# Kernel optimization log

Measured on AMD Instinct MI355X. Metric: run time of the kernel, lower is better.

The kernel has to match this reference:

```python
import jax, jax.numpy as jnp
import numpy as np

EPS = 1e-8  # EPSILON in original repo (sharpen denom); cosine eps matches torch default 1e-8
MAX_SHIFT = 1
M_FEAT = 128


def _lstm_cell(x, h, c, W_ih, W_hh, b_ih, b_hh):
    gates = x @ W_ih.T + b_ih + h @ W_hh.T + b_hh
    i, f, g, o = jnp.split(gates, 4, axis=1)
    c_new = jax.nn.sigmoid(f) * c + jax.nn.sigmoid(i) * jnp.tanh(g)
    h_new = jax.nn.sigmoid(o) * jnp.tanh(c_new)
    return h_new, c_new


def _content_address(bank, k, b):
    # torch cosine_similarity over dim 2: dot / max(|m||k|, eps)
    dot = jnp.einsum('bnm,bm->bn', bank, k)
    denom = jnp.maximum(jnp.linalg.norm(bank, axis=2) * jnp.linalg.norm(k, axis=1, keepdims=True), 1e-8)
    return jax.nn.softmax(b * dot / denom, axis=1)


def _shift(w, s):
    # circular unroll then valid cross-correlation with per-batch kernel s [B, 2*MAX_SHIFT+1]
    wp = jnp.concatenate([w[:, -MAX_SHIFT:], w, w[:, :MAX_SHIFT]], axis=1)
    N = w.shape[1]
    taps = 2 * MAX_SHIFT + 1
    return sum(s[:, i:i + 1] * wp[:, i:i + N] for i in range(taps))


def _sharpen(w, r):
    wr = w ** r
    return wr / (wr.sum(axis=1, keepdims=True) + EPS)


def _move(bank, w_prev, k, b, g, s, r):
    w = _content_address(bank, k, b)
    w = w + (1.0 - g) * w_prev  # faithful: w_c is NOT scaled by g in the source
    w = _shift(w, s)
    return _sharpen(w, r)


def _split_read(p):
    M = M_FEAT
    k = p[:, :M]
    b = jax.nn.softplus(p[:, M:M + 1])
    g = jax.nn.sigmoid(p[:, M + 1:M + 2])
    s = jax.nn.softmax(p[:, M + 2:M + 5], axis=1)
    r = 1.0 + jax.nn.softplus(p[:, M + 5:M + 6])
    return k, b, g, s, r


def _split_write(p):
    M = M_FEAT
    k, b, g, s, r = _split_read(p[:, :M + 6])
    e = jax.nn.sigmoid(p[:, M + 6:M + 6 + M])
    a = p[:, M + 6 + M:M + 6 + 2 * M]
    return k, b, g, s, r, e, a


def setup_inputs() -> dict:
    key = jax.random.key(0)
    ks = jax.random.split(key, 16)
    B, E, H, N, M, O = 64, 256, 512, 4096, 128, 256
    rd_out, wr_out = M + 2 * MAX_SHIFT + 4, 3 * M + 2 * MAX_SHIFT + 4
    sc = 0.05
    return {
        'x': jax.random.normal(ks[0], (B, E), jnp.float32),
        'h_prev': jax.random.normal(ks[1], (B, H), jnp.float32),
        'c_prev': jax.random.normal(ks[2], (B, H), jnp.float32),
        'bank': jax.random.normal(ks[3], (B, N, M), jnp.float32) * 0.1,
        'read_w_prev': jnp.zeros((3, B, N), jnp.float32),
        'write_w_prev': jnp.zeros((3, B, N), jnp.float32),
        'W_ih': jax.random.normal(ks[4], (4 * H, E), jnp.float32) * sc,
        'W_hh': jax.random.normal(ks[5], (4 * H, H), jnp.float32) * sc,
        'b_ih': jax.random.normal(ks[6], (4 * H,), jnp.float32) * sc,
        'b_hh': jax.random.normal(ks[7], (4 * H,), jnp.float32) * sc,
        'read_W': jax.random.normal(ks[8], (3, rd_out, H), jnp.float32) * sc,
        'read_b': jax.random.normal(ks[9], (3, rd_out), jnp.float32) * sc,
        'write_W': jax.random.normal(ks[10], (3, wr_out, H), jnp.float32) * sc,
        'write_b': jax.random.normal(ks[11], (3, wr_out), jnp.float32) * sc,
        'out_W': jax.random.normal(ks[12], (O, 3 * M + H), jnp.float32) * sc,
        'out_b': jax.random.normal(ks[13], (O,), jnp.float32) * sc,
    }


def reference(x, h_prev, c_prev, bank, read_w_prev, write_w_prev,
              W_ih, W_hh, b_ih, b_hh, read_W, read_b, write_W, write_b,
              out_W, out_b):
    h, c = _lstm_cell(x, h_prev, c_prev, W_ih, W_hh, b_ih, b_hh)
    reads = []
    for i in range(3):  # head_num=3, structurally distinct params per head
        # write head: update bank
        pw = h @ write_W[i].T + write_b[i]
        k, b, g, s, r, e, a = _split_write(pw)
        ww = _move(bank, write_w_prev[i], k, b, g, s, r)
        bank = bank * (1.0 - ww[:, :, None] * e[:, None, :]) + ww[:, :, None] * a[:, None, :]
        # read head: read from updated bank
        pr = h @ read_W[i].T + read_b[i]
        k, b, g, s, r = _split_read(pr)
        wr = _move(bank, read_w_prev[i], k, b, g, s, r)
        reads.append(jnp.einsum('bn,bnm->bm', wr, bank))
    out = jnp.concatenate(reads + [h], axis=1) @ out_W.T + out_b
    return out
```

## Files before the change

### kernel.cpp

```cpp
#include <hip/hip_runtime.h>
#include <math.h>

namespace {

constexpr int kB = 64;
constexpr int kN = 4096;
constexpr int kM = 128;
constexpr int kH = 512;
constexpr int kE = 256;
constexpr int kO = 256;
constexpr int kGates = 4 * kH;
constexpr int kCatW = 3 * kM + kH;
constexpr int kPRow = 1600;
constexpr int kWN = kB * kN;
constexpr int GRID = 256;
constexpr int TPB = 512;
constexpr float kLog2e = 1.4426950408889634f;

__device__ __forceinline__ float sigm_(float x) { return 1.f / (1.f + expf(-x)); }
__device__ __forceinline__ float softplus_(float x) { return x > 20.f ? x : log1pf(expf(x)); }

struct Args {
  const float *x, *h_prev, *c_prev, *bank, *read_w_prev, *write_w_prev;
  const float *W_ih, *W_hh, *b_ih, *b_hh, *read_W, *read_b, *write_W, *write_b, *out_W, *out_b;
  float *out;
  float *gates0, *gates1, *praw0, *praw1, *cat;
  float *kwb, *krb, *evb, *avb, *scal, *sdot;
  float *wp0, *wp1, *wp2, *wp3, *wp4, *wp5;
  float *mA, *mB;
  unsigned *cnt;
};

union SMem {
  struct { float At[64 * 20]; float Wt[64 * 65]; } g;
  struct { float hs[256 * 18]; float Wt[64 * 65]; } p;
  struct { float wb[kN]; float red[8]; } a;
  struct { float nred[4][2]; } s;
  struct { float rl[2 * kM]; } r;
  struct { float As[64 * 72]; float Ws[64 * 72]; } o;
};

__device__ __forceinline__ void gsync(unsigned* cnt, unsigned target) {
  __syncthreads();
  if (threadIdx.x == 0) {
    __builtin_amdgcn_fence(__ATOMIC_RELEASE, "agent");
    __hip_atomic_fetch_add(cnt, 1u, __ATOMIC_RELAXED, __HIP_MEMORY_SCOPE_AGENT);
    while (__hip_atomic_load(cnt, __ATOMIC_RELAXED, __HIP_MEMORY_SCOPE_AGENT) < target)
      __builtin_amdgcn_s_sleep(1);
    __builtin_amdgcn_fence(__ATOMIC_ACQUIRE, "agent");
  }
  __syncthreads();
}

__device__ void addr_core8(int tid, float* loc, const float* sc, const float* __restrict__ wp,
                           float* wb, float* red) {
  const float g = sc[1], r = sc[2];
  const float s0 = sc[3], s1c = sc[4], s2 = sc[5];
  const int lane = tid & 63, wid = tid >> 6;
  __syncthreads();
  float mx = loc[0];
#pragma unroll
  for (int i = 1; i < 8; i++) mx = fmaxf(mx, loc[i]);
#pragma unroll
  for (int m = 1; m < 64; m <<= 1) mx = fmaxf(mx, __shfl_xor(mx, m, 64));
  if (lane == 0) red[wid] = mx;
  __syncthreads();
  mx = red[0];
#pragma unroll
  for (int k = 1; k < 8; k++) mx = fmaxf(mx, red[k]);
  float sum = 0.f;
#pragma unroll
  for (int i = 0; i < 8; i++) { loc[i] = exp2f((loc[i] - mx) * kLog2e); sum += loc[i]; }
#pragma unroll
  for (int m = 1; m < 64; m <<= 1) sum += __shfl_xor(sum, m, 64);
  __syncthreads();
  if (lane == 0) red[wid] = sum;
  __syncthreads();
  sum = red[0];
#pragma unroll
  for (int k = 1; k < 8; k++) sum += red[k];
  const float inv = 1.f / sum;
  const float omg = 1.f - g;
#pragma unroll
  for (int i = 0; i < 8; i++) {
    int n = tid + i * TPB;
    wb[n] = loc[i] * inv + omg * wp[n];
  }
  __syncthreads();
  float ssum = 0.f;
#pragma unroll
  for (int i = 0; i < 8; i++) {
    int n = tid + i * TPB;
    float sh = s0 * wb[(n + kN - 1) & (kN - 1)] + s1c * wb[n] + s2 * wb[(n + 1) & (kN - 1)];
    float y = (sh > 0.f) ? exp2f(r * log2f(sh)) : 0.f;
    loc[i] = y;
    ssum += y;
  }
#pragma unroll
  for (int m = 1; m < 64; m <<= 1) ssum += __shfl_xor(ssum, m, 64);
  __syncthreads();
  if (lane == 0) red[wid] = ssum;
  __syncthreads();
  ssum = red[0];
#pragma unroll
  for (int k = 1; k < 8; k++) ssum += red[k];
  const float invs = 1.f / (ssum + 1e-8f);
#pragma unroll
  for (int i = 0; i < 8; i++) loc[i] *= invs;
  __syncthreads();
}

__global__ __launch_bounds__(TPB, 2) void mega(Args P) {
  const int bid = blockIdx.x;
  const int tid = threadIdx.x;
  __shared__ SMem sm;

  {
    const int khalf = bid >> 7;
    const int unit = bid & 127;
    const int b0 = (unit >> 5) * 16;
    const int j0 = (unit & 31) * 64;
    const int jg = tid & 63;
    const int bq2 = (tid >> 6) * 2;
    float acc0 = 0.f, acc1 = 0.f;
    for (int kc6 = 0; kc6 < 6; kc6++) {
      const int kc = khalf * 6 + kc6;
      const bool isx = kc < 4;
      const float* A = isx ? P.x : P.h_prev;
      const float* W = isx ? P.W_ih : P.W_hh;
      const int lda = isx ? kE : kH;
      const int k0 = (isx ? kc : (kc - 4)) * 64;
      __syncthreads();
      {
        int bb = tid >> 5;
        int kk = (tid & 31) * 2;
        float2 v = *(const float2*)(A + (size_t)(b0 + bb) * lda + k0 + kk);
        sm.g.At[(kk + 0) * 20 + bb] = v.x;
        sm.g.At[(kk + 1) * 20 + bb] = v.y;
      }
#pragma unroll
      for (int i = 0; i < 2; i++) {
        int idx = tid + i * 512;
        int jj = idx >> 4;
        int kk = (idx & 15) * 4;
        float4 w = *(const float4*)(W + (size_t)(j0 + jj) * lda + k0 + kk);
        sm.g.Wt[(kk + 0) * 65 + jj] = w.x; sm.g.Wt[(kk + 1) * 65 + jj] = w.y;
        sm.g.Wt[(kk + 2) * 65 + jj] = w.z; sm.g.Wt[(kk + 3) * 65 + jj] = w.w;
      }
      __syncthreads();
#pragma unroll 4
      for (int k = 0; k < 64; k++) {
        float2 av = *(const float2*)&sm.g.At[k * 20 + bq2];
        float wv = sm.g.Wt[k * 65 + jg];
        acc0 += av.x * wv; acc1 += av.y * wv;
      }
    }
    float* gd = khalf ? P.gates1 : P.gates0;
    gd[(size_t)(b0 + bq2 + 0) * kGates + j0 + jg] = acc0;
    gd[(size_t)(b0 + bq2 + 1) * kGates + j0 + jg] = acc1;
  }
  gsync(P.cnt, GRID * 1);

  if (bid < 200) {
    const int kh = bid / 100;
    const int u = bid % 100;
    const int b0 = (u / 25) * 16;
    const int jt = u % 25;
    const int j0 = jt * 64;
    const int kbase = kh * 256;
    for (int i = tid; i < 16 * 256; i += TPB) {
      int bb = i >> 8, kl = i & 255;
      int kk = kbase + kl;
      int b = b0 + bb;
      const float* g0 = P.gates0 + (size_t)b * kGates;
      const float* g1 = P.gates1 + (size_t)b * kGates;
      float i_ = g0[kk]        + g1[kk]        + P.b_ih[kk]        + P.b_hh[kk];
      float f_ = g0[512 + kk]  + g1[512 + kk]  + P.b_ih[512 + kk]  + P.b_hh[512 + kk];
      float gg = g0[1024 + kk] + g1[1024 + kk] + P.b_ih[1024 + kk] + P.b_hh[1024 + kk];
      float o_ = g0[1536 + kk] + g1[1536 + kk] + P.b_ih[1536 + kk] + P.b_hh[1536 + kk];
      float c = sigm_(f_) * P.c_prev[(size_t)b * kH + kk] + sigm_(i_) * tanhf(gg);
      float h = sigm_(o_) * tanhf(c);
      sm.p.hs[kl * 18 + bb] = h;
      if (jt == 0) P.cat[(size_t)b * kCatW + 3 * kM + kk] = h;
    }
    const int jg = tid & 63;
    const int bq2 = (tid >> 6) * 2;
    float acc0 = 0.f, acc1 = 0.f;
    for (int kc = 0; kc < 4; kc++) {
      const int k0 = kbase + kc * 64;
      const int kl0 = kc * 64;
      __syncthreads();
#pragma unroll
      for (int i = 0; i < 2; i++) {
        int idx = tid + i * 512;
        int jj = idx >> 4;
        int kk = (idx & 15) * 4;
        int j = j0 + jj;
        float4 w = make_float4(0.f, 0.f, 0.f, 0.f);
        if (j < 1170)      w = *(const float4*)(P.write_W + (size_t)j * kH + k0 + kk);
        else if (j < 1572) w = *(const float4*)(P.read_W + (size_t)(j - 1170) * kH + k0 + kk);
        sm.p.Wt[(kk + 0) * 65 + jj] = w.x; sm.p.Wt[(kk + 1) * 65 + jj] = w.y;
        sm.p.Wt[(kk + 2) * 65 + jj] = w.z; sm.p.Wt[(kk + 3) * 65 + jj] = w.w;
      }
      __syncthreads();
#pragma unroll 4
      for (int k = 0; k < 64; k++) {
        float2 av = *(const float2*)&sm.p.hs[(kl0 + k) * 18 + bq2];
        float wv = sm.p.Wt[k * 65 + jg];
        acc0 += av.x * wv; acc1 += av.y * wv;
      }
    }
    float* pd = kh ? P.praw1 : P.praw0;
    if (j0 + jg < 1572) {
      pd[(size_t)(b0 + bq2 + 0) * kPRow + j0 + jg] = acc0;
      pd[(size_t)(b0 + bq2 + 1) * kPRow + j0 + jg] = acc1;
    }
  } else if (bid < 216) {
#pragma unroll
    for (int q = 0; q < 2; q++) {
      int i = (bid - 200) * 1024 + tid + q * 512;
      P.out[i] = P.out_b[i & (kO - 1)];
    }
  } else if (bid < 232) {
#pragma unroll
    for (int q = 0; q < 3; q++) {
      int i = (bid - 216) * 1536 + tid + q * 512;
      P.cat[(size_t)(i / 384) * kCatW + (i % 384)] = 0.f;
    }
  }
  gsync(P.cnt, GRID * 2);

  if (bid < kB) {
    const int b = bid;
    const int m = tid & 127;
    const int hg = tid >> 7;
    const float* pr0 = P.praw0 + (size_t)b * kPRow;
    const float* pr1 = P.praw1 + (size_t)b * kPRow;
    {
      const bool isw = hg < 3;
      const int base = isw ? hg * 390 : 1170;
      const float* bias = isw ? (P.write_b + hg * 390) : P.read_b;
      const int slot = isw ? hg : 3;
      float kv = pr0[base + m] + pr1[base + m] + bias[m];
      if (isw) {
        P.kwb[((size_t)hg * kB + b) * kM + m] = kv;
        P.evb[((size_t)hg * kB + b) * kM + m] =
            sigm_(pr0[base + 134 + m] + pr1[base + 134 + m] + bias[134 + m]);
        P.avb[((size_t)hg * kB + b) * kM + m] =
            pr0[base + 262 + m] + pr1[base + 262 + m] + bias[262 + m];
      } else {
        P.krb[((size_t)0 * kB + b) * kM + m] = kv;
      }
      float sq = kv * kv;
#pragma unroll
      for (int mm = 1; mm < 64; mm <<= 1) sq += __shfl_xor(sq, mm, 64);
      if ((tid & 63) == 0) sm.s.nred[hg][m >> 6] = sq;
      __syncthreads();
      if (m == 0) {
        float* s = P.scal + ((size_t)slot * kB + b) * 8;
        s[0] = softplus_(pr0[base + 128] + pr1[base + 128] + bias[128]);
        s[1] = sigm_(pr0[base + 129] + pr1[base + 129] + bias[129]);
        s[2] = 1.f + softplus_(pr0[base + 133] + pr1[base + 133] + bias[133]);
        float x0 = pr0[base + 130] + pr1[base + 130] + bias[130];
        float x1 = pr0[base + 131] + pr1[base + 131] + bias[131];
        float x2 = pr0[base + 132] + pr1[base + 132] + bias[132];
        float mx = fmaxf(x0, fmaxf(x1, x2));
        float e0 = expf(x0 - mx), e1 = expf(x1 - mx), e2 = expf(x2 - mx);
        float si = 1.f / (e0 + e1 + e2);
        s[3] = e0 * si; s[4] = e1 * si; s[5] = e2 * si;
        s[6] = sqrtf(sm.s.nred[hg][0] + sm.s.nred[hg][1]);
      }
      __syncthreads();
    }
    {
      const int j = (hg < 2) ? hg + 1 : 2;
      const bool act = hg < 2;
      const int base = 1170 + j * 134;
      const float* bias = P.read_b + j * 134;
      const int slot = 3 + j;
      float kv = pr0[base + m] + pr1[base + m] + bias[m];
      if (act) P.krb[((size_t)j * kB + b) * kM + m] = kv;
      float sq = kv * kv;
#pragma unroll
      for (int mm = 1; mm < 64; mm <<= 1) sq += __shfl_xor(sq, mm, 64);
      if ((tid & 63) == 0) sm.s.nred[hg][m >> 6] = sq;
      __syncthreads();
      if (m == 0 && act) {
        float* s = P.scal + ((size_t)slot * kB + b) * 8;
        s[0] = softplus_(pr0[base + 128] + pr1[base + 128] + bias[128]);
        s[1] = sigm_(pr0[base + 129] + pr1[base + 129] + bias[129]);
        s[2] = 1.f + softplus_(pr0[base + 133] + pr1[base + 133] + bias[133]);
        float x0 = pr0[base + 130] + pr1[base + 130] + bias[130];
        float x1 = pr0[base + 131] + pr1[base + 131] + bias[131];
        float x2 = pr0[base + 132] + pr1[base + 132] + bias[132];
        float mx = fmaxf(x0, fmaxf(x1, x2));
        float e0 = expf(x0 - mx), e1 = expf(x1 - mx), e2 = expf(x2 - mx);
        float si = 1.f / (e0 + e1 + e2);
        s[3] = e0 * si; s[4] = e1 * si; s[5] = e2 * si;
        s[6] = sqrtf(sm.s.nred[hg][0] + sm.s.nred[hg][1]);
      }
      __syncthreads();
    }
    if (tid < 64) {
      const float* a0v = P.avb + ((size_t)0 * kB + b) * kM;
      const float* a2v = P.avb + ((size_t)2 * kB + b) * kM;
      const float* u[5] = {a0v, a0v, a0v, a2v, a2v};
      const float* v[5] = {P.krb + ((size_t)0 * kB + b) * kM,
                           P.kwb + ((size_t)1 * kB + b) * kM,
                           a0v,
                           P.krb + ((size_t)2 * kB + b) * kM,
                           a2v};
#pragma unroll
      for (int d = 0; d < 5; d++) {
        float s = u[d][tid] * v[d][tid] + u[d][tid + 64] * v[d][tid + 64];
#pragma unroll
        for (int mm = 1; mm < 64; mm <<= 1) s += __shfl_xor(s, mm, 64);
        if (tid == 0) P.sdot[b * 8 + d] = s;
      }
    }
  }
  gsync(P.cnt, GRID * 3);

  {
    const int b = bid >> 2, chunk = bid & 3;
    const int lane = tid & 63, wv = tid >> 6, sub = lane >> 4, lm = lane & 15;
    const int m8 = lm * 8;
    float kw0r[8], kr0r[8], kw1r[8], a0r[8], e0r[8];
#pragma unroll
    for (int t = 0; t < 8; t++) {
      kw0r[t] = P.kwb[((size_t)0 * kB + b) * kM + m8 + t];
      kr0r[t] = P.krb[((size_t)0 * kB + b) * kM + m8 + t];
      kw1r[t] = P.kwb[((size_t)1 * kB + b) * kM + m8 + t];
      a0r[t]  = P.avb[((size_t)0 * kB + b) * kM + m8 + t];
      e0r[t]  = P.evb[((size_t)0 * kB + b) * kM + m8 + t];
    }
    const size_t bbase = (size_t)b * kN * kM;
    const size_t brow = (size_t)b * kN;
    const int row0 = chunk * 1024 + wv * 4 + sub;
    const float* base = P.bank + bbase + (size_t)row0 * kM + m8;
    float4 pA0 = *(const float4*)(base);
    float4 pA1 = *(const float4*)(base + 4);
    float4 pB0 = *(const float4*)(base + (size_t)32 * kM);
    float4 pB1 = *(const float4*)(base + (size_t)32 * kM + 4);
    for (int it = 0; it < 32; it++) {
      float v[8];
      if ((it & 1) == 0) {
        v[0]=pA0.x; v[1]=pA0.y; v[2]=pA0.z; v[3]=pA0.w; v[4]=pA1.x; v[5]=pA1.y; v[6]=pA1.z; v[7]=pA1.w;
        if (it + 2 < 32) {
          const float* np = base + (size_t)(it + 2) * 32 * kM;
          pA0 = *(const float4*)np; pA1 = *(const float4*)(np + 4);
        }
      } else {
        v[0]=pB0.x; v[1]=pB0.y; v[2]=pB0.z; v[3]=pB0.w; v[4]=pB1.x; v[5]=pB1.y; v[6]=pB1.z; v[7]=pB1.w;
        if (it + 2 < 32) {
          const float* np = base + (size_t)(it + 2) * 32 * kM;
          pB0 = *(const float4*)np; pB1 = *(const float4*)(np + 4);
        }
      }
      const int row = row0 + it * 32;
      float s[10] = {};
#pragma unroll
      for (int t = 0; t < 8; t++) {
        float be = v[t] * e0r[t];
        s[0] += v[t] * kw0r[t];
        s[1] += v[t] * v[t];
        s[2] += v[t] * kr0r[t];
        s[3] += be * kr0r[t];
        s[4] += v[t] * kw1r[t];
        s[5] += be * kw1r[t];
        s[6] += be * v[t];
        s[7] += be * be;
        s[8] += v[t] * a0r[t];
        s[9] += be * a0r[t];
      }
#pragma unroll
      for (int m = 1; m < 16; m <<= 1)
#pragma unroll
        for (int k = 0; k < 10; k++) s[k] += __shfl_xor(s[k], m, 64);
      if (lm == 0) {
        float4* dst = (float4*)(P.mA + (size_t)(brow + row) * 12);
        dst[0] = make_float4(s[0], s[1], s[2], s[3]);
        dst[1] = make_float4(s[4], s[5], s[6], s[7]);
        dst[2] = make_float4(s[8], s[9], 0.f, 0.f);
      }
    }
  }
  gsync(P.cnt, GRID * 4);

  if (bid < 2 * kB) {
    const int b = bid & 63, role = bid >> 6;
    const size_t brow = (size_t)b * kN;
    float loc[8], w0r[8];
    {
      const float* sc = P.scal + ((size_t)0 * kB + b) * 8;
      const float beta = sc[0], kn = sc[6];
#pragma unroll
      for (int i = 0; i < 8; i++) {
        const float* mp = P.mA + (size_t)(brow + tid + i * TPB) * 12;
        float4 q0 = *(const float4*)mp;
        loc[i] = beta * q0.x / fmaxf(sqrtf(fmaxf(q0.y, 0.f)) * kn, 1e-8f);
      }
      addr_core8(tid, loc, sc, P.write_w_prev + brow, sm.a.wb, sm.a.red);
#pragma unroll
      for (int i = 0; i < 8; i++) {
        w0r[i] = loc[i];
        if (role == 0) P.wp0[brow + tid + i * TPB] = loc[i];
      }
    }
    if (role == 0) {
      const float* sc = P.scal + ((size_t)3 * kB + b) * 8;
      const float beta = sc[0], kn = sc[6];
      const float sa0kr0 = P.sdot[b * 8 + 0], sa0a0 = P.sdot[b * 8 + 2];
#pragma unroll
      for (int i = 0; i < 8; i++) {
        const float* mp = P.mA + (size_t)(brow + tid + i * TPB) * 12;
        float4 q0 = *(const float4*)mp;
        float4 q1 = *(const float4*)(mp + 4);
        float4 q2 = *(const float4*)(mp + 8);
        float w0 = w0r[i], w0q = w0 * w0;
        float q1v = q0.y - 2.f * w0 * q1.z + w0q * q1.w + 2.f * w0 * q2.x
                  - 2.f * w0q * q2.y + w0q * sa0a0;
        float d = q0.z - w0 * q0.w + w0 * sa0kr0;
        loc[i] = beta * d / fmaxf(sqrtf(fmaxf(q1v, 0.f)) * kn, 1e-8f);
      }
      addr_core8(tid, loc, sc, P.read_w_prev + brow, sm.a.wb, sm.a.red);
#pragma unroll
      for (int i = 0; i < 8; i++) P.wp2[brow + tid + i * TPB] = loc[i];
    } else {
      const float* sc = P.scal + ((size_t)1 * kB + b) * 8;
      const float beta = sc[0], kn = sc[6];
      const float sa0kw1 = P.sdot[b * 8 + 1], sa0a0 = P.sdot[b * 8 + 2];
#pragma unroll
      for (int i = 0; i < 8; i++) {
        const float* mp = P.mA + (size_t)(brow + tid + i * TPB) * 12;
        float4 q0 = *(const float4*)mp;
        float4 q1 = *(const float4*)(mp + 4);
        float4 q2 = *(const float4*)(mp + 8);
        float w0 = w0r[i], w0q = w0 * w0;
        float q1v = q0.y - 2.f * w0 * q1.z + w0q * q1.w + 2.f * w0 * q2.x
                  - 2.f * w0q * q2.y + w0q * sa0a0;
        float d = q1.x - w0 * q1.y + w0 * sa0kw1;
        loc[i] = beta * d / fmaxf(sqrtf(fmaxf(q1v, 0.f)) * kn, 1e-8f);
      }
      addr_core8(tid, loc, sc, P.write_w_prev + (size_t)kWN + brow, sm.a.wb, sm.a.red);
#pragma unroll
      for (int i = 0; i < 8; i++) P.wp1[brow + tid + i * TPB] = loc[i];
    }
  }
  gsync(P.cnt, GRID * 5);

  {
    const int b = bid >> 2, chunk = bid & 3;
    const int lane = tid & 63, wv = tid >> 6, sub = lane >> 4, lm = lane & 15;
    const int m8 = lm * 8;
    float e0r[8], a0r[8], e1r[8], a1r[8], kr1r[8], kw2r[8], kr2r[8], e2r[8], a2r[8];
#pragma unroll
    for (int t = 0; t < 8; t++) {
      e0r[t]  = P.evb[((size_t)0 * kB + b) * kM + m8 + t];
      a0r[t]  = P.avb[((size_t)0 * kB + b) * kM + m8 + t];
      e1r[t]  = P.evb[((size_t)1 * kB + b) * kM + m8 + t];
      a1r[t]  = P.avb[((size_t)1 * kB + b) * kM + m8 + t];
      kr1r[t] = P.krb[((size_t)1 * kB + b) * kM + m8 + t];
      kw2r[t] = P.kwb[((size_t)2 * kB + b) * kM + m8 + t];
      kr2r[t] = P.krb[((size_t)2 * kB + b) * kM + m8 + t];
      e2r[t]  = P.evb[((size_t)2 * kB + b) * kM + m8 + t];
      a2r[t]  = P.avb[((size_t)2 * kB + b) * kM + m8 + t];
    }
    float racc[8] = {};
    if (tid < kM) sm.r.rl[tid] = 0.f;
    const size_t bbase = (size_t)b * kN * kM;
    const size_t brow = (size_t)b * kN;
    const int row0 = chunk * 1024 + wv * 4 + sub;
    const float* base = P.bank + bbase + (size_t)row0 * kM + m8;
    const size_t wrow = brow + row0;
    float4 pA0 = *(const float4*)(base);
    float4 pA1 = *(const float4*)(base + 4);
    float4 pB0 = *(const float4*)(base + (size_t)32 * kM);
    float4 pB1 = *(const float4*)(base + (size_t)32 * kM + 4);
    float w0A = P.wp0[wrow], w1A = P.wp1[wrow], r0A = P.wp2[wrow];
    float w0B = P.wp0[wrow + 32], w1B = P.wp1[wrow + 32], r0B = P.wp2[wrow + 32];
    for (int it = 0; it < 32; it++) {
      float v[8];
      float w0, w1, wr0;
      if ((it & 1) == 0) {
        v[0]=pA0.x; v[1]=pA0.y; v[2]=pA0.z; v[3]=pA0.w; v[4]=pA1.x; v[5]=pA1.y; v[6]=pA1.z; v[7]=pA1.w;
        w0 = w0A; w1 = w1A; wr0 = r0A;
        if (it + 2 < 32) {
          const float* np = base + (size_t)(it + 2) * 32 * kM;
          pA0 = *(const float4*)np; pA1 = *(const float4*)(np + 4);
          size_t wn = wrow + (size_t)(it + 2) * 32;
          w0A = P.wp0[wn]; w1A = P.wp1[wn]; r0A = P.wp2[wn];
        }
      } else {
        v[0]=pB0.x; v[1]=pB0.y; v[2]=pB0.z; v[3]=pB0.w; v[4]=pB1.x; v[5]=pB1.y; v[6]=pB1.z; v[7]=pB1.w;
        w0 = w0B; w1 = w1B; wr0 = r0B;
        if (it + 2 < 32) {
          const float* np = base + (size_t)(it + 2) * 32 * kM;
          pB0 = *(const float4*)np; pB1 = *(const float4*)(np + 4);
          size_t wn = wrow + (size_t)(it + 2) * 32;
          w0B = P.wp0[wn]; w1B = P.wp1[wn]; r0B = P.wp2[wn];
        }
      }
      const int row = row0 + it * 32;
#pragma unroll
      for (int t = 0; t < 8; t++) {
        v[t] += w0 * (a0r[t] - e0r[t] * v[t]);
        racc[t] += wr0 * v[t];
        v[t] += w1 * (a1r[t] - e1r[t] * v[t]);
      }
      float s[9] = {};
#pragma unroll
      for (int t = 0; t < 8; t++) {
        float ve = v[t] * e2r[t];
        s[0] += v[t] * kr1r[t];
        s[1] += v[t] * kw2r[t];
        s[2] += v[t] * v[t];
        s[3] += v[t] * kr2r[t];
        s[4] += ve * kr2r[t];
        s[5] += ve * v[t];
        s[6] += ve * ve;
        s[7] += v[t] * a2r[t];
        s[8] += ve * a2r[t];
      }
#pragma unroll
      for (int m = 1; m < 16; m <<= 1)
#pragma unroll
        for (int k = 0; k < 9; k++) s[k] += __shfl_xor(s[k], m, 64);
      if (lm == 0) {
        float4* dst = (float4*)(P.mB + (size_t)(brow + row) * 12);
        dst[0] = make_float4(s[0], s[1], s[2], s[3]);
        dst[1] = make_float4(s[4], s[5], s[6], s[7]);
        dst[2] = make_float4(s[8], 0.f, 0.f, 0.f);
      }
    }
    __syncthreads();
#pragma unroll
    for (int t = 0; t < 8; t++) {
      racc[t] += __shfl_xor(racc[t], 16, 64);
      racc[t] += __shfl_xor(racc[t], 32, 64);
    }
    if (sub == 0) {
#pragma unroll
      for (int t = 0; t < 8; t++) atomicAdd(&sm.r.rl[m8 + t], racc[t]);
    }
    __syncthreads();
    if (tid < kM) atomicAdd(&P.cat[(size_t)b * kCatW + tid], sm.r.rl[tid]);
  }
  gsync(P.cnt, GRID * 6);

  if (bid < 2 * kB) {
    const int b = bid & 63, role = bid >> 6;
    const size_t brow = (size_t)b * kN;
    float loc[8];
    if (role == 0) {
      float w2r[8];
      {
        const float* sc = P.scal + ((size_t)2 * kB + b) * 8;
        const float beta = sc[0], kn = sc[6];
#pragma unroll
        for (int i = 0; i < 8; i++) {
          const float* mp = P.mB + (size_t)(brow + tid + i * TPB) * 12;
          float4 q0 = *(const float4*)mp;
          loc[i] = beta * q0.y / fmaxf(sqrtf(fmaxf(q0.z, 0.f)) * kn, 1e-8f);
        }
        addr_core8(tid, loc, sc, P.write_w_prev + (size_t)2 * kWN + brow, sm.a.wb, sm.a.red);
#pragma unroll
        for (int i = 0; i < 8; i++) {
          P.wp3[brow + tid + i * TPB] = loc[i];
          w2r[i] = loc[i];
        }
      }
      {
        const float* sc = P.scal + ((size_t)5 * kB + b) * 8;
        const float beta = sc[0], kn = sc[6];
        const float sa2kr2 = P.sdot[b * 8 + 3], sa2a2 = P.sdot[b * 8 + 4];
#pragma unroll
        for (int i = 0; i < 8; i++) {
          const float* mp = P.mB + (size_t)(brow + tid + i * TPB) * 12;
          float4 q0 = *(const float4*)mp;
          float4 q1 = *(const float4*)(mp + 4);
          float4 q2 = *(const float4*)(mp + 8);
          float w2 = w2r[i], w2q = w2 * w2;
          float q3 = q0.z - 2.f * w2 * q1.y + w2q * q1.z + 2.f * w2 * q1.w
                   - 2.f * w2q * q2.x + w2q * sa2a2;
          float d = q0.w - w2 * q1.x + w2 * sa2kr2;
          loc[i] = beta * d / fmaxf(sqrtf(fmaxf(q3, 0.f)) * kn, 1e-8f);
        }
        addr_core8(tid, loc, sc, P.read_w_prev + (size_t)2 * kWN + brow, sm.a.wb, sm.a.red);
#pragma unroll
        for (int i = 0; i < 8; i++) P.wp5[brow + tid + i * TPB] = loc[i];
      }
    } else {
      {
        const float* sc = P.scal + ((size_t)4 * kB + b) * 8;
        const float beta = sc[0], kn = sc[6];
#pragma unroll
        for (int i = 0; i < 8; i++) {
          const float* mp = P.mB + (size_t)(brow + tid + i * TPB) * 12;
          float4 q0 = *(const float4*)mp;
          loc[i] = beta * q0.x / fmaxf(sqrtf(fmaxf(q0.z, 0.f)) * kn, 1e-8f);
        }
        addr_core8(tid, loc, sc, P.read_w_prev + (size_t)kWN + brow, sm.a.wb, sm.a.red);
#pragma unroll
        for (int i = 0; i < 8; i++) P.wp4[brow + tid + i * TPB] = loc[i];
      }
    }
  }
  gsync(P.cnt, GRID * 7);

  {
    const int b = bid >> 2, chunk = bid & 3;
    const int lane = tid & 63, wv = tid >> 6, sub = lane >> 4, lm = lane & 15;
    const int m8 = lm * 8;
    float e_r[3][8], a_r[3][8];
#pragma unroll
    for (int j = 0; j < 3; j++)
#pragma unroll
      for (int t = 0; t < 8; t++) {
        e_r[j][t] = P.evb[((size_t)j * kB + b) * kM + m8 + t];
        a_r[j][t] = P.avb[((size_t)j * kB + b) * kM + m8 + t];
      }
    float racc1[8] = {}, racc2[8] = {};
    if (tid < kM) { sm.r.rl[tid] = 0.f; sm.r.rl[kM + tid] = 0.f; }
    const size_t bbase = (size_t)b * kN * kM;
    const size_t brow = (size_t)b * kN;
    const int row0 = chunk * 1024 + wv * 4 + sub;
    const float* base = P.bank + bbase + (size_t)row0 * kM + m8;
    const size_t wrow = brow + row0;
    float4 pA0 = *(const float4*)(base);
    float4 pA1 = *(const float4*)(base + 4);
    float4 pB0 = *(const float4*)(base + (size_t)32 * kM);
    float4 pB1 = *(const float4*)(base + (size_t)32 * kM + 4);
    float c0A = P.wp0[wrow], c1A = P.wp1[wrow], c2A = P.wp3[wrow], c3A = P.wp4[wrow], c4A = P.wp5[wrow];
    float c0B = P.wp0[wrow + 32], c1B = P.wp1[wrow + 32], c2B = P.wp3[wrow + 32],
          c3B = P.wp4[wrow + 32], c4B = P.wp5[wrow + 32];
    for (int it = 0; it < 32; it++) {
      float v[8];
      float w0, w1, w2, wr1, wr2;
      if ((it & 1) == 0) {
        v[0]=pA0.x; v[1]=pA0.y; v[2]=pA0.z; v[3]=pA0.w; v[4]=pA1.x; v[5]=pA1.y; v[6]=pA1.z; v[7]=pA1.w;
        w0 = c0A; w1 = c1A; w2 = c2A; wr1 = c3A; wr2 = c4A;
        if (it + 2 < 32) {
          const float* np = base + (size_t)(it + 2) * 32 * kM;
          pA0 = *(const float4*)np; pA1 = *(const float4*)(np + 4);
          size_t wn = wrow + (size_t)(it + 2) * 32;
          c0A = P.wp0[wn]; c1A = P.wp1[wn]; c2A = P.wp3[wn]; c3A = P.wp4[wn]; c4A = P.wp5[wn];
        }
      } else {
        v[0]=pB0.x; v[1]=pB0.y; v[2]=pB0.z; v[3]=pB0.w; v[4]=pB1.x; v[5]=pB1.y; v[6]=pB1.z; v[7]=pB1.w;
        w0 = c0B; w1 = c1B; w2 = c2B; wr1 = c3B; wr2 = c4B;
        if (it + 2 < 32) {
          const float* np = base + (size_t)(it + 2) * 32 * kM;
          pB0 = *(const float4*)np; pB1 = *(const float4*)(np + 4);
          size_t wn = wrow + (size_t)(it + 2) * 32;
          c0B = P.wp0[wn]; c1B = P.wp1[wn]; c2B = P.wp3[wn]; c3B = P.wp4[wn]; c4B = P.wp5[wn];
        }
      }
#pragma unroll
      for (int t = 0; t < 8; t++) {
        v[t] += w0 * (a_r[0][t] - e_r[0][t] * v[t]);
        v[t] += w1 * (a_r[1][t] - e_r[1][t] * v[t]);
        racc1[t] += wr1 * v[t];
        v[t] += w2 * (a_r[2][t] - e_r[2][t] * v[t]);
        racc2[t] += wr2 * v[t];
      }
    }
    __syncthreads();
#pragma unroll
    for (int t = 0; t < 8; t++) {
      racc1[t] += __shfl_xor(racc1[t], 16, 64);
      racc1[t] += __shfl_xor(racc1[t], 32, 64);
      racc2[t] += __shfl_xor(racc2[t], 16, 64);
      racc2[t] += __shfl_xor(racc2[t], 32, 64);
    }
    if (sub == 0) {
#pragma unroll
      for (int t = 0; t < 8; t++) {
        atomicAdd(&sm.r.rl[m8 + t], racc1[t]);
        atomicAdd(&sm.r.rl[kM + m8 + t], racc2[t]);
      }
    }
    __syncthreads();
    if (tid < kM) {
      atomicAdd(&P.cat[(size_t)b * kCatW + kM + tid], sm.r.rl[tid]);
      atomicAdd(&P.cat[(size_t)b * kCatW + 2 * kM + tid], sm.r.rl[kM + tid]);
    }
  }
  gsync(P.cnt, GRID * 8);

  if (bid < 56) {
    const int jt = bid & 3, kt = bid >> 2;
    const int j0 = jt * 64, k0 = kt * 64;
    {
      int bb = tid >> 3;
      int kk = (tid & 7) * 8;
      float4 v0 = *(const float4*)(P.cat + (size_t)bb * kCatW + k0 + kk);
      float4 v1 = *(const float4*)(P.cat + (size_t)bb * kCatW + k0 + kk + 4);
      sm.o.As[(kk + 0) * 72 + bb] = v0.x; sm.o.As[(kk + 1) * 72 + bb] = v0.y;
      sm.o.As[(kk + 2) * 72 + bb] = v0.z; sm.o.As[(kk + 3) * 72 + bb] = v0.w;
      sm.o.As[(kk + 4) * 72 + bb] = v1.x; sm.o.As[(kk + 5) * 72 + bb] = v1.y;
      sm.o.As[(kk + 6) * 72 + bb] = v1.z; sm.o.As[(kk + 7) * 72 + bb] = v1.w;
      float4 w0_ = *(const float4*)(P.out_W + (size_t)(j0 + bb) * kCatW + k0 + kk);
      float4 w1_ = *(const float4*)(P.out_W + (size_t)(j0 + bb) * kCatW + k0 + kk + 4);
      sm.o.Ws[(kk + 0) * 72 + bb] = w0_.x; sm.o.Ws[(kk + 1) * 72 + bb] = w0_.y;
      sm.o.Ws[(kk + 2) * 72 + bb] = w0_.z; sm.o.Ws[(kk + 3) * 72 + bb] = w0_.w;
      sm.o.Ws[(kk + 4) * 72 + bb] = w1_.x; sm.o.Ws[(kk + 5) * 72 + bb] = w1_.y;
      sm.o.Ws[(kk + 6) * 72 + bb] = w1_.z; sm.o.Ws[(kk + 7) * 72 + bb] = w1_.w;
    }
    __syncthreads();
    const int b0 = (tid & 15) * 4;
    const int jq = (tid >> 4) * 2;
    float acc[4][2] = {};
#pragma unroll 2
    for (int k = 0; k < 64; k++) {
      float4 av = *(const float4*)&sm.o.As[k * 72 + b0];
      float2 wv = *(const float2*)&sm.o.Ws[k * 72 + jq];
      acc[0][0] += av.x * wv.x; acc[0][1] += av.x * wv.y;
      acc[1][0] += av.y * wv.x; acc[1][1] += av.y * wv.y;
      acc[2][0] += av.z * wv.x; acc[2][1] += av.z * wv.y;
      acc[3][0] += av.w * wv.x; acc[3][1] += av.w * wv.y;
    }
#pragma unroll
    for (int ii = 0; ii < 4; ii++) {
      atomicAdd(&P.out[(size_t)(b0 + ii) * kO + j0 + jq + 0], acc[ii][0]);
      atomicAdd(&P.out[(size_t)(b0 + ii) * kO + j0 + jq + 1], acc[ii][1]);
    }
  }
}

}

extern "C" void kernel_launch(void* const* d_in, const int* in_sizes, int n_in,
                              void* d_out, int out_size, void* d_ws, size_t ws_size,
                              hipStream_t stream) {
  Args A_;
  A_.x            = (const float*)d_in[0];
  A_.h_prev       = (const float*)d_in[1];
  A_.c_prev       = (const float*)d_in[2];
  A_.bank         = (const float*)d_in[3];
  A_.read_w_prev  = (const float*)d_in[4];
  A_.write_w_prev = (const float*)d_in[5];
  A_.W_ih         = (const float*)d_in[6];
  A_.W_hh         = (const float*)d_in[7];
  A_.b_ih         = (const float*)d_in[8];
  A_.b_hh         = (const float*)d_in[9];
  A_.read_W       = (const float*)d_in[10];
  A_.read_b       = (const float*)d_in[11];
  A_.write_W      = (const float*)d_in[12];
  A_.write_b      = (const float*)d_in[13];
  A_.out_W        = (const float*)d_in[14];
  A_.out_b        = (const float*)d_in[15];
  A_.out = (float*)d_out;

  float* ws = (float*)d_ws;
  A_.cnt = (unsigned*)d_ws;
  float* p = ws + 64;
  A_.gates0 = p; p += (size_t)kB * kGates;
  A_.gates1 = p; p += (size_t)kB * kGates;
  A_.praw0  = p; p += (size_t)kB * kPRow;
  A_.praw1  = p; p += (size_t)kB * kPRow;
  A_.cat    = p; p += (size_t)kB * kCatW;
  A_.kwb    = p; p += (size_t)3 * kB * kM;
  A_.krb    = p; p += (size_t)3 * kB * kM;
  A_.evb    = p; p += (size_t)3 * kB * kM;
  A_.avb    = p; p += (size_t)3 * kB * kM;
  A_.scal   = p; p += (size_t)6 * kB * 8;
  A_.sdot   = p; p += (size_t)kB * 8;
  A_.wp0    = p; p += (size_t)kWN;
  A_.wp1    = p; p += (size_t)kWN;
  A_.wp2    = p; p += (size_t)kWN;
  A_.wp3    = p; p += (size_t)kWN;
  A_.wp4    = p; p += (size_t)kWN;
  A_.wp5    = p; p += (size_t)kWN;
  A_.mA     = p; p += (size_t)kWN * 12;
  A_.mB     = p; p += (size_t)kWN * 12;

  hipMemsetAsync(d_ws, 0, 256, stream);
  mega<<<dim3(GRID), dim3(TPB), 0, stream>>>(A_);

  (void)in_sizes; (void)n_in; (void)out_size; (void)ws_size;
}
```

Measured before the change: 490.9 us.

## Replace grid-wide barriers with per-batch barriers and fuse output GEMM per batch

```diff
diff --git a/kernel.cpp b/kernel.cpp
--- a/kernel.cpp
+++ b/kernel.cpp
@@ -28,7 +28,8 @@
   float *kwb, *krb, *evb, *avb, *scal, *sdot;
   float *wp0, *wp1, *wp2, *wp3, *wp4, *wp5;
   float *mA, *mB;
-  unsigned *cnt;
+  unsigned *gcnt;
+  unsigned *bcnt;
 };
 
 union SMem {
@@ -37,15 +38,14 @@
   struct { float wb[kN]; float red[8]; } a;
   struct { float nred[4][2]; } s;
   struct { float rl[2 * kM]; } r;
-  struct { float As[64 * 72]; float Ws[64 * 72]; } o;
 };
 
-__device__ __forceinline__ void gsync(unsigned* cnt, unsigned target) {
+__device__ __forceinline__ void barrier_on(unsigned* c, unsigned target) {
   __syncthreads();
   if (threadIdx.x == 0) {
     __builtin_amdgcn_fence(__ATOMIC_RELEASE, "agent");
-    __hip_atomic_fetch_add(cnt, 1u, __ATOMIC_RELAXED, __HIP_MEMORY_SCOPE_AGENT);
-    while (__hip_atomic_load(cnt, __ATOMIC_RELAXED, __HIP_MEMORY_SCOPE_AGENT) < target)
+    __hip_atomic_fetch_add(c, 1u, __ATOMIC_RELAXED, __HIP_MEMORY_SCOPE_AGENT);
+    while (__hip_atomic_load(c, __ATOMIC_RELAXED, __HIP_MEMORY_SCOPE_AGENT) < target)
       __builtin_amdgcn_s_sleep(1);
     __builtin_amdgcn_fence(__ATOMIC_ACQUIRE, "agent");
   }
@@ -114,6 +114,10 @@
   const int bid = blockIdx.x;
   const int tid = threadIdx.x;
   __shared__ SMem sm;
+
+  const int bb_ = bid & 63;
+  const int sub_ = bid >> 6;
+  unsigned* bc = P.bcnt + bb_ * 32;
 
   {
     const int khalf = bid >> 7;
@@ -159,7 +163,7 @@
     gd[(size_t)(b0 + bq2 + 0) * kGates + j0 + jg] = acc0;
     gd[(size_t)(b0 + bq2 + 1) * kGates + j0 + jg] = acc1;
   }
-  gsync(P.cnt, GRID * 1);
+  barrier_on(P.gcnt, GRID * 1);
 
   if (bid < 200) {
     const int kh = bid / 100;
@@ -215,27 +219,18 @@
       pd[(size_t)(b0 + bq2 + 0) * kPRow + j0 + jg] = acc0;
       pd[(size_t)(b0 + bq2 + 1) * kPRow + j0 + jg] = acc1;
     }
-  } else if (bid < 216) {
-#pragma unroll
-    for (int q = 0; q < 2; q++) {
-      int i = (bid - 200) * 1024 + tid + q * 512;
-      P.out[i] = P.out_b[i & (kO - 1)];
-    }
-  } else if (bid < 232) {
-#pragma unroll
-    for (int q = 0; q < 3; q++) {
-      int i = (bid - 216) * 1536 + tid + q * 512;
-      P.cat[(size_t)(i / 384) * kCatW + (i % 384)] = 0.f;
-    }
-  }
-  gsync(P.cnt, GRID * 2);
-
-  if (bid < kB) {
-    const int b = bid;
+  }
+  barrier_on(P.gcnt, GRID * 2);
+
+  const int b = bb_;
+  const size_t brow = (size_t)b * kN;
+
+  if (sub_ == 0) {
     const int m = tid & 127;
     const int hg = tid >> 7;
     const float* pr0 = P.praw0 + (size_t)b * kPRow;
     const float* pr1 = P.praw1 + (size_t)b * kPRow;
+    if (tid < 384) P.cat[(size_t)b * kCatW + tid] = 0.f;
     {
       const bool isw = hg < 3;
       const int base = isw ? hg * 390 : 1170;
@@ -319,10 +314,10 @@
       }
     }
   }
-  gsync(P.cnt, GRID * 3);
+  barrier_on(bc, 4);
 
   {
-    const int b = bid >> 2, chunk = bid & 3;
+    const int chunk = sub_;
     const int lane = tid & 63, wv = tid >> 6, sub = lane >> 4, lm = lane & 15;
     const int m8 = lm * 8;
     float kw0r[8], kr0r[8], kw1r[8], a0r[8], e0r[8];
@@ -335,7 +330,6 @@
       e0r[t]  = P.evb[((size_t)0 * kB + b) * kM + m8 + t];
     }
     const size_t bbase = (size_t)b * kN * kM;
-    const size_t brow = (size_t)b * kN;
     const int row0 = chunk * 1024 + wv * 4 + sub;
     const float* base = P.bank + bbase + (size_t)row0 * kM + m8;
     float4 pA0 = *(const float4*)(base);
@@ -385,11 +379,10 @@
       }
     }
   }
-  gsync(P.cnt, GRID * 4);
-
-  if (bid < 2 * kB) {
-    const int b = bid & 63, role = bid >> 6;
-    const size_t brow = (size_t)b * kN;
+  barrier_on(bc, 8);
+
+  if (sub_ < 2) {
+    const int role = sub_;
     float loc[8], w0r[8];
     {
       const float* sc = P.scal + ((size_t)0 * kB + b) * 8;
@@ -447,10 +440,10 @@
       for (int i = 0; i < 8; i++) P.wp1[brow + tid + i * TPB] = loc[i];
     }
   }
-  gsync(P.cnt, GRID * 5);
+  barrier_on(bc, 12);
 
   {
-    const int b = bid >> 2, chunk = bid & 3;
+    const int chunk = sub_;
     const int lane = tid & 63, wv = tid >> 6, sub = lane >> 4, lm = lane & 15;
     const int m8 = lm * 8;
     float e0r[8], a0r[8], e1r[8], a1r[8], kr1r[8], kw2r[8], kr2r[8], e2r[8], a2r[8];
@@ -469,7 +462,6 @@
     float racc[8] = {};
     if (tid < kM) sm.r.rl[tid] = 0.f;
     const size_t bbase = (size_t)b * kN * kM;
-    const size_t brow = (size_t)b * kN;
     const int row0 = chunk * 1024 + wv * 4 + sub;
     const float* base = P.bank + bbase + (size_t)row0 * kM + m8;
     const size_t wrow = brow + row0;
@@ -546,11 +538,10 @@
     __syncthreads();
     if (tid < kM) atomicAdd(&P.cat[(size_t)b * kCatW + tid], sm.r.rl[tid]);
   }
-  gsync(P.cnt, GRID * 6);
-
-  if (bid < 2 * kB) {
-    const int b = bid & 63, role = bid >> 6;
-    const size_t brow = (size_t)b * kN;
+  barrier_on(bc, 16);
+
+  if (sub_ < 2) {
+    const int role = sub_;
     float loc[8];
     if (role == 0) {
       float w2r[8];
@@ -606,10 +597,10 @@
       }
     }
   }
-  gsync(P.cnt, GRID * 7);
+  barrier_on(bc, 20);
 
   {
-    const int b = bid >> 2, chunk = bid & 3;
+    const int chunk = sub_;
     const int lane = tid & 63, wv = tid >> 6, sub = lane >> 4, lm = lane & 15;
     const int m8 = lm * 8;
     float e_r[3][8], a_r[3][8];
@@ -623,7 +614,6 @@
     float racc1[8] = {}, racc2[8] = {};
     if (tid < kM) { sm.r.rl[tid] = 0.f; sm.r.rl[kM + tid] = 0.f; }
     const size_t bbase = (size_t)b * kN * kM;
-    const size_t brow = (size_t)b * kN;
     const int row0 = chunk * 1024 + wv * 4 + sub;
     const float* base = P.bank + bbase + (size_t)row0 * kM + m8;
     const size_t wrow = brow + row0;
@@ -686,45 +676,24 @@
       atomicAdd(&P.cat[(size_t)b * kCatW + 2 * kM + tid], sm.r.rl[kM + tid]);
     }
   }
-  gsync(P.cnt, GRID * 8);
-
-  if (bid < 56) {
-    const int jt = bid & 3, kt = bid >> 2;
-    const int j0 = jt * 64, k0 = kt * 64;
-    {
-      int bb = tid >> 3;
-      int kk = (tid & 7) * 8;
-      float4 v0 = *(const float4*)(P.cat + (size_t)bb * kCatW + k0 + kk);
-      float4 v1 = *(const float4*)(P.cat + (size_t)bb * kCatW + k0 + kk + 4);
-      sm.o.As[(kk + 0) * 72 + bb] = v0.x; sm.o.As[(kk + 1) * 72 + bb] = v0.y;
-      sm.o.As[(kk + 2) * 72 + bb] = v0.z; sm.o.As[(kk + 3) * 72 + bb] = v0.w;
-      sm.o.As[(kk + 4) * 72 + bb] = v1.x; sm.o.As[(kk + 5) * 72 + bb] = v1.y;
-      sm.o.As[(kk + 6) * 72 + bb] = v1.z; sm.o.As[(kk + 7) * 72 + bb] = v1.w;
-      float4 w0_ = *(const float4*)(P.out_W + (size_t)(j0 + bb) * kCatW + k0 + kk);
-      float4 w1_ = *(const float4*)(P.out_W + (size_t)(j0 + bb) * kCatW + k0 + kk + 4);
-      sm.o.Ws[(kk + 0) * 72 + bb] = w0_.x; sm.o.Ws[(kk + 1) * 72 + bb] = w0_.y;
-      sm.o.Ws[(kk + 2) * 72 + bb] = w0_.z; sm.o.Ws[(kk + 3) * 72 + bb] = w0_.w;
-      sm.o.Ws[(kk + 4) * 72 + bb] = w1_.x; sm.o.Ws[(kk + 5) * 72 + bb] = w1_.y;
-      sm.o.Ws[(kk + 6) * 72 + bb] = w1_.z; sm.o.Ws[(kk + 7) * 72 + bb] = w1_.w;
-    }
-    __syncthreads();
-    const int b0 = (tid & 15) * 4;
-    const int jq = (tid >> 4) * 2;
-    float acc[4][2] = {};
-#pragma unroll 2
-    for (int k = 0; k < 64; k++) {
-      float4 av = *(const float4*)&sm.o.As[k * 72 + b0];
-      float2 wv = *(const float2*)&sm.o.Ws[k * 72 + jq];
-      acc[0][0] += av.x * wv.x; acc[0][1] += av.x * wv.y;
-      acc[1][0] += av.y * wv.x; acc[1][1] += av.y * wv.y;
-      acc[2][0] += av.z * wv.x; acc[2][1] += av.z * wv.y;
-      acc[3][0] += av.w * wv.x; acc[3][1] += av.w * wv.y;
-    }
-#pragma unroll
-    for (int ii = 0; ii < 4; ii++) {
-      atomicAdd(&P.out[(size_t)(b0 + ii) * kO + j0 + jq + 0], acc[ii][0]);
-      atomicAdd(&P.out[(size_t)(b0 + ii) * kO + j0 + jq + 1], acc[ii][1]);
-    }
+  barrier_on(bc, 24);
+
+  {
+    const int j = sub_ * 64 + (tid >> 3);
+    const int ks = (tid & 7) * 112;
+    const float* crow = P.cat + (size_t)b * kCatW;
+    const float* wrow = P.out_W + (size_t)j * kCatW;
+    float acc = 0.f;
+#pragma unroll 7
+    for (int k = 0; k < 112; k += 4) {
+      float4 cv = *(const float4*)(crow + ks + k);
+      float4 wv = *(const float4*)(wrow + ks + k);
+      acc += cv.x * wv.x + cv.y * wv.y + cv.z * wv.z + cv.w * wv.w;
+    }
+    acc += __shfl_xor(acc, 1, 64);
+    acc += __shfl_xor(acc, 2, 64);
+    acc += __shfl_xor(acc, 4, 64);
+    if ((tid & 7) == 0) P.out[(size_t)b * kO + j] = P.out_b[j] + acc;
   }
 }
 
@@ -753,8 +722,9 @@
   A_.out = (float*)d_out;
 
   float* ws = (float*)d_ws;
-  A_.cnt = (unsigned*)d_ws;
-  float* p = ws + 64;
+  A_.gcnt = (unsigned*)d_ws;
+  A_.bcnt = (unsigned*)d_ws + 64;
+  float* p = ws + 4096;
   A_.gates0 = p; p += (size_t)kB * kGates;
   A_.gates1 = p; p += (size_t)kB * kGates;
   A_.praw0  = p; p += (size_t)kB * kPRow;
@@ -775,7 +745,7 @@
   A_.mA     = p; p += (size_t)kWN * 12;
   A_.mB     = p; p += (size_t)kWN * 12;
 
-  hipMemsetAsync(d_ws, 0, 256, stream);
+  hipMemsetAsync(d_ws, 0, 16384, stream);
   mega<<<dim3(GRID), dim3(TPB), 0, stream>>>(A_);
 
   (void)in_sizes; (void)n_in; (void)out_size; (void)ws_size;
```

Result: faster. 430.8 us (-12.3%).
